# Performance work log

Hardware: AMD Instinct MI355X
Metric: run time of the kernel (lower is better)

## Reference

```python
import jax, jax.numpy as jnp
import numpy as np

COS_EPS = 1e-8  # torch F.cosine_similarity eps


def setup_inputs() -> dict:
    key = jax.random.key(0)
    k1, k2 = jax.random.split(key)
    x = jax.random.normal(k1, (8192, 512), dtype=jnp.float32)
    class_logits = jax.random.normal(k2, (8192, 100), dtype=jnp.float32)
    return {"x": x, "class_logits": class_logits}


def reference(x, class_logits):
    N, D = x.shape
    C = class_logits.shape[1]

    # class_logits.clone().detach()
    logits = jax.lax.stop_gradient(class_logits)
    pred = jax.nn.softmax(logits, axis=1)
    max_logit = pred.max(axis=1)          # [N]
    max_cls = pred.argmax(axis=1)         # [N] int

    # graph(): pairwise cosine similarity = normalize rows + gram matmul
    norms = jnp.linalg.norm(x, axis=1, keepdims=True)
    xn = x / jnp.maximum(norms, COS_EPS)
    mat = xn @ xn.T                       # [N, N]

    x_agg = mat @ x + x                   # [N, D]
    x_new = jax.lax.stop_gradient(x_agg)

    # update_prototype: per-class weighted scatter-add then mean over counts
    weighted = x_new * max_logit[:, None]                     # [N, D]
    sums = jax.ops.segment_sum(weighted, max_cls, num_segments=C)      # [C, D]
    counts = jax.ops.segment_sum(jnp.ones((N,), x.dtype), max_cls, num_segments=C)  # [C]
    prototypes = jnp.where(counts[:, None] > 0,
                           sums / jnp.maximum(counts, 1.0)[:, None],
                           jnp.zeros_like(sums))              # [C, D]

    # inter_class_matrix[i, j] = prototypes[j] - prototypes[i]
    inter_class_matrix = prototypes[None, :, :] - prototypes[:, None, :]  # [C, C, D]
    return prototypes, inter_class_matrix
```

## Files before the change

### kernel.cpp

```cpp
#include <hip/hip_runtime.h>
#include <math.h>

#define N_ROWS 8192
#define D_DIM  512
#define C_CLS  100

typedef unsigned short u16;
typedef unsigned int u32;
typedef __attribute__((ext_vector_type(8))) short short8;
typedef __attribute__((ext_vector_type(4))) float floatx4;

#define WS_G      0
#define WS_GP     262144
#define WS_INV    5505024
#define WS_SINV   5513216
#define WS_WV     5521408
#define WS_CLS    5529600
#define WS_CNT    5537792
#define WS_OFFS   5537920
#define WS_ORDER  5538048
#define WS_ZTH    5546240
#define WS_ZTL    7643392
#define WS_U      9740544
#define WS_V      9791744

__device__ __forceinline__ void split2(float v, u16& h, u16& l) {
    unsigned u = __float_as_uint(v);
    h = (u16)(u >> 16);
    float r = v - __uint_as_float(u & 0xFFFF0000u);
    l = (u16)(__float_as_uint(r) >> 16);
}

typedef const __attribute__((address_space(1))) u32* gp32;
typedef __attribute__((address_space(3))) u32* lp32;
__device__ __forceinline__ void cp16(const u16* g, u16* l) {
    __builtin_amdgcn_global_load_lds((gp32)g, (lp32)l, 16, 0, 0);
}

__global__ __launch_bounds__(256) void k_prep(const float* __restrict__ logits,
        const float* __restrict__ x, float* __restrict__ wv,
        int* __restrict__ cls, float* __restrict__ inv, float* __restrict__ sinv) {
    int wave = (blockIdx.x * blockDim.x + threadIdx.x) >> 6;
    int lane = threadIdx.x & 63;
    if (wave >= N_ROWS) return;
    const float* row = logits + (size_t)wave * C_CLS;
    float v1 = row[lane];
    bool has2 = (lane + 64) < C_CLS;
    float v2 = has2 ? row[lane + 64] : -INFINITY;
    float m; int idx;
    if (v2 > v1) { m = v2; idx = lane + 64; } else { m = v1; idx = lane; }
    #pragma unroll
    for (int off = 32; off >= 1; off >>= 1) {
        float om = __shfl_down(m, off);
        int   oi = __shfl_down(idx, off);
        if (om > m || (om == m && oi < idx)) { m = om; idx = oi; }
    }
    m = __shfl(m, 0);
    idx = __shfl(idx, 0);
    float s = expf(v1 - m) + (has2 ? expf(v2 - m) : 0.0f);
    #pragma unroll
    for (int off = 32; off >= 1; off >>= 1) s += __shfl_down(s, off);
    const float* xr = x + (size_t)wave * D_DIM;
    float ss = 0.f;
    #pragma unroll
    for (int j = 0; j < D_DIM; j += 64) {
        float v = xr[j + lane];
        ss += v * v;
    }
    #pragma unroll
    for (int off = 32; off >= 1; off >>= 1) ss += __shfl_down(ss, off);
    if (lane == 0) {
        wv[wave] = 1.0f / s;
        cls[wave] = idx;
        float iv = 1.0f / fmaxf(sqrtf(ss), 1e-8f);
        inv[wave] = iv;
        sinv[wave] = sqrtf(iv);
    }
}

#define LDT 65
__global__ __launch_bounds__(256) void k_mid(const float* __restrict__ x,
        const float* __restrict__ sinv, const int* __restrict__ cls,
        u16* __restrict__ zth, u16* __restrict__ ztl,
        int* __restrict__ cnt, int* __restrict__ offs, int* __restrict__ order) {
    __shared__ unsigned zt_p[64 * LDT];
    int bx = blockIdx.x;
    int t = threadIdx.x;
    if (bx == 1024) {
        __shared__ int hist[128], scan_s[128], cur[128];
        if (t < 128) hist[t] = 0;
        __syncthreads();
        for (int m2 = t; m2 < N_ROWS; m2 += 256) atomicAdd(&hist[cls[m2]], 1);
        __syncthreads();
        if (t < 128) scan_s[t] = hist[t];
        __syncthreads();
        #pragma unroll
        for (int d = 1; d < 128; d <<= 1) {
            int add = 0;
            if (t < 128 && t >= d) add = scan_s[t - d];
            __syncthreads();
            if (t < 128) scan_s[t] += add;
            __syncthreads();
        }
        if (t < 128) {
            int off0 = scan_s[t] - hist[t];
            cur[t] = off0;
            offs[t] = off0;
            cnt[t] = hist[t];
        }
        __syncthreads();
        for (int m2 = t; m2 < N_ROWS; m2 += 256) {
            int c2 = cls[m2];
            int p = atomicAdd(&cur[c2], 1);
            order[p] = m2;
        }
        return;
    }
    int r0 = (bx & 127) << 6, c0 = (bx >> 7) << 6;
    int r = t >> 2, cq = t & 3;
    const float* src = x + (size_t)(r0 + r) * D_DIM + c0 + cq * 16;
    float vv[16];
    {
        float4 a = *(const float4*)(src + 0);
        float4 b = *(const float4*)(src + 4);
        float4 c = *(const float4*)(src + 8);
        float4 d = *(const float4*)(src + 12);
        vv[0]=a.x; vv[1]=a.y; vv[2]=a.z; vv[3]=a.w;
        vv[4]=b.x; vv[5]=b.y; vv[6]=b.z; vv[7]=b.w;
        vv[8]=c.x; vv[9]=c.y; vv[10]=c.z; vv[11]=c.w;
        vv[12]=d.x; vv[13]=d.y; vv[14]=d.z; vv[15]=d.w;
    }
    float sv = sinv[r0 + r];
    #pragma unroll
    for (int j = 0; j < 16; ++j) {
        u16 h, l;
        split2(sv * vv[j], h, l);
        zt_p[(cq * 16 + j) * LDT + r] = ((unsigned)h << 16) | l;
    }
    __syncthreads();
    int c = t >> 2, rq = (t & 3) * 16;
    size_t tbase = (size_t)(c0 + c) * N_ROWS + r0 + rq;
    uint oh[8], ol[8];
    #pragma unroll
    for (int p = 0; p < 8; ++p) {
        unsigned d0 = zt_p[c * LDT + rq + 2*p];
        unsigned d1 = zt_p[c * LDT + rq + 2*p + 1];
        oh[p] = (d0 >> 16) | (d1 & 0xFFFF0000u);
        ol[p] = (d0 & 0xFFFFu) | (d1 << 16);
    }
    *(uint4*)&zth[tbase]     = make_uint4(oh[0], oh[1], oh[2], oh[3]);
    *(uint4*)&zth[tbase + 8] = make_uint4(oh[4], oh[5], oh[6], oh[7]);
    *(uint4*)&ztl[tbase]     = make_uint4(ol[0], ol[1], ol[2], ol[3]);
    *(uint4*)&ztl[tbase + 8] = make_uint4(ol[4], ol[5], ol[6], ol[7]);
}

__global__ __launch_bounds__(256) void k_big(const u16* __restrict__ zth,
        const u16* __restrict__ ztl, const float* __restrict__ x,
        const float* __restrict__ inv, const float* __restrict__ wv,
        const int* __restrict__ order, const int* __restrict__ offs,
        const int* __restrict__ cnt, float* __restrict__ Gp,
        float* __restrict__ u, float* __restrict__ v) {
    __shared__ __attribute__((aligned(16))) u16 Ah[128*32], Al[128*32];
    __shared__ __attribute__((aligned(16))) u16 Bh[128*32], Bl[128*32];
    __shared__ float us[4][64], vs[4][64];
    int bx = blockIdx.x;
    int t = threadIdx.x;
    if (bx >= 320) {
        int idx = bx - 320;
        int c = idx >> 3, jc = idx & 7;
        int g = t >> 6, lane = t & 63;
        int j = jc * 64 + lane;
        int n = cnt[c], o = offs[c];
        float ua = 0.f, va = 0.f;
        for (int p = g; p < n; p += 4) {
            int m = order[o + p];
            float wm = wv[m];
            float wi = wm * inv[m];
            float xv = x[(size_t)m * D_DIM + j];
            ua += wi * xv; va += wm * xv;
        }
        us[g][lane] = ua; vs[g][lane] = va;
        __syncthreads();
        if (g == 0) {
            u[(size_t)c * D_DIM + j] = us[0][lane] + us[1][lane] + us[2][lane] + us[3][lane];
            v[(size_t)c * D_DIM + j] = vs[0][lane] + vs[1][lane] + vs[2][lane] + vs[3][lane];
        }
        return;
    }
    int tile = bx % 10;
    int p = bx / 10;
    int ti = tile < 4 ? 0 : (tile < 7 ? 1 : (tile < 9 ? 2 : 3));
    int tj = tile - (ti == 0 ? 0 : (ti == 1 ? 3 : (ti == 2 ? 5 : 6)));
    int i0 = ti << 7, j0 = tj << 7;
    bool diag = (ti == tj);
    int kb = p << 8;
    int w = t >> 6, l = t & 63;
    int srow = t >> 2, scol = (t & 3) << 3;
    int lm = l & 15, lg = l >> 4;
    floatx4 acc[4][4];
    #pragma unroll
    for (int mi = 0; mi < 4; ++mi)
        #pragma unroll
        for (int ni = 0; ni < 4; ++ni) acc[mi][ni] = (floatx4){0.f,0.f,0.f,0.f};
    int d0 = srow * 32 + scol;
    int d1 = (64 + srow) * 32 + scol;
    const size_t ga0 = (size_t)(i0 + srow) * N_ROWS + kb + scol;
    const size_t ga1 = (size_t)(i0 + 64 + srow) * N_ROWS + kb + scol;
    const size_t gb0 = (size_t)(j0 + srow) * N_ROWS + kb + scol;
    const size_t gb1 = (size_t)(j0 + 64 + srow) * N_ROWS + kb + scol;
    const u16* Bhs = diag ? Ah : Bh;
    const u16* Bls = diag ? Al : Bl;
    for (int s = 0; s < 8; ++s) {
        int ks = s << 5;
        cp16(zth + ga0 + ks, Ah + d0);
        cp16(zth + ga1 + ks, Ah + d1);
        cp16(ztl + ga0 + ks, Al + d0);
        cp16(ztl + ga1 + ks, Al + d1);
        if (!diag) {
            cp16(zth + gb0 + ks, Bh + d0);
            cp16(zth + gb1 + ks, Bh + d1);
            cp16(ztl + gb0 + ks, Bl + d0);
            cp16(ztl + gb1 + ks, Bl + d1);
        }
        __syncthreads();
        short8 ah[4], al[4], bh[4], bl[4];
        #pragma unroll
        for (int mi = 0; mi < 4; ++mi) {
            int off = (((w & 1) << 6) + (mi << 4) + lm) * 32 + (lg << 3);
            ah[mi] = *(const short8*)&Ah[off];
            al[mi] = *(const short8*)&Al[off];
        }
        #pragma unroll
        for (int ni = 0; ni < 4; ++ni) {
            int off = (((w >> 1) << 6) + (ni << 4) + lm) * 32 + (lg << 3);
            bh[ni] = *(const short8*)&Bhs[off];
            bl[ni] = *(const short8*)&Bls[off];
        }
        #pragma unroll
        for (int mi = 0; mi < 4; ++mi)
            #pragma unroll
            for (int ni = 0; ni < 4; ++ni) {
                acc[mi][ni] = __builtin_amdgcn_mfma_f32_16x16x32_bf16(ah[mi], bh[ni], acc[mi][ni], 0, 0, 0);
                acc[mi][ni] = __builtin_amdgcn_mfma_f32_16x16x32_bf16(ah[mi], bl[ni], acc[mi][ni], 0, 0, 0);
                acc[mi][ni] = __builtin_amdgcn_mfma_f32_16x16x32_bf16(al[mi], bh[ni], acc[mi][ni], 0, 0, 0);
            }
        __syncthreads();
    }
    float* Gb = Gp + ((size_t)(p * 10 + tile) << 14);
    #pragma unroll
    for (int mi = 0; mi < 4; ++mi) {
        int row0 = ((w & 1) << 6) + (mi << 4) + (lg << 2);
        #pragma unroll
        for (int ni = 0; ni < 4; ++ni) {
            int col = ((w >> 1) << 6) + (ni << 4) + lm;
            #pragma unroll
            for (int r = 0; r < 4; ++r)
                Gb[(size_t)(row0 + r) * 128 + col] = acc[mi][ni][r];
        }
    }
}

__global__ void k_reduceG(const float* __restrict__ Gp, float* __restrict__ G) {
    int i = blockIdx.x * 256 + threadIdx.x;
    int r = i >> 9, c = i & 511;
    int tr = r >> 7, tc = c >> 7, rr = r & 127, cc = c & 127;
    if (tr > tc) { int tmp = tr; tr = tc; tc = tmp; tmp = rr; rr = cc; cc = tmp; }
    int tid = tr * 4 + tc - ((tr * (tr + 1)) >> 1);
    const float* src = Gp + ((size_t)tid << 14) + rr * 128 + cc;
    float s = 0.f;
    #pragma unroll
    for (int p = 0; p < 32; ++p) s += src[(size_t)p * 163840];
    G[i] = s;
}

__global__ __launch_bounds__(256) void k_pgemm(const float* __restrict__ u,
        const float* __restrict__ v, const int* __restrict__ cnt,
        const float* __restrict__ G, float* __restrict__ out) {
    __shared__ float us[D_DIM];
    int c = blockIdx.x >> 1;
    int j = ((blockIdx.x & 1) << 8) + threadIdx.x;
    us[threadIdx.x]       = u[(size_t)c * D_DIM + threadIdx.x];
    us[threadIdx.x + 256] = u[(size_t)c * D_DIM + threadIdx.x + 256];
    __syncthreads();
    float acc = v[(size_t)c * D_DIM + j];
    #pragma unroll 8
    for (int k = 0; k < D_DIM; ++k)
        acc += us[k] * G[(size_t)k * D_DIM + j];
    int n = cnt[c];
    float s = (n > 0) ? 1.0f / (float)n : 0.0f;
    out[(size_t)c * D_DIM + j] = acc * s;
}

__global__ void k_inter(const float* __restrict__ proto, float* __restrict__ out) {
    int pair = blockIdx.x;
    int i = pair / C_CLS;
    int j = pair - i * C_CLS;
    int d = threadIdx.x << 2;
    float4 pj = *(const float4*)&proto[j * D_DIM + d];
    float4 pi = *(const float4*)&proto[i * D_DIM + d];
    float4 r;
    r.x = pj.x - pi.x; r.y = pj.y - pi.y; r.z = pj.z - pi.z; r.w = pj.w - pi.w;
    *(float4*)&out[(size_t)pair * D_DIM + d] = r;
}

extern "C" void kernel_launch(void* const* d_in, const int* in_sizes, int n_in,
                              void* d_out, int out_size, void* d_ws, size_t ws_size,
                              hipStream_t stream) {
    const float* x      = (const float*)d_in[0];
    const float* logits = (const float*)d_in[1];
    float* out = (float*)d_out;
    float* ws  = (float*)d_ws;
    float* G     = ws + WS_G;
    float* Gp    = ws + WS_GP;
    float* inv   = ws + WS_INV;
    float* sinv  = ws + WS_SINV;
    float* wv    = ws + WS_WV;
    int*   cls   = (int*)(ws + WS_CLS);
    int*   cnt   = (int*)(ws + WS_CNT);
    int*   offs  = (int*)(ws + WS_OFFS);
    int*   order = (int*)(ws + WS_ORDER);
    u16* zth = (u16*)(ws + WS_ZTH);
    u16* ztl = (u16*)(ws + WS_ZTL);
    float* u_arr = ws + WS_U;
    float* v_arr = ws + WS_V;

    k_prep<<<N_ROWS / 4, 256, 0, stream>>>(logits, x, wv, cls, inv, sinv);
    k_mid<<<1025, 256, 0, stream>>>(x, sinv, cls, zth, ztl, cnt, offs, order);
    k_big<<<1120, 256, 0, stream>>>(zth, ztl, x, inv, wv, order, offs, cnt, Gp, u_arr, v_arr);
    k_reduceG<<<D_DIM * D_DIM / 256, 256, 0, stream>>>(Gp, G);
    k_pgemm<<<C_CLS * 2, 256, 0, stream>>>(u_arr, v_arr, cnt, G, out);
    k_inter<<<C_CLS * C_CLS, 128, 0, stream>>>(out, out + C_CLS * D_DIM);
}
```

Baseline: 178.8 us.

## Fuse all phases into one cooperative persistent kernel with grid syncs

Merges the six separate kernel launches into a single cooperative kernel of 256 persistent blocks that runs each phase in turn, separated by grid-wide syncs, with shared memory reused through a union. The Gram split-K is halved from 32 to 16 partitions, so each block does twice the K-work and the reduction reads fewer partials. The aim is to remove launch gaps and tail effects between the kernels. The cost is far less parallelism: the 1120-block GEMM becomes 160 MFMA blocks on a GPU with 256 CUs, and grid.sync adds its own overhead. A fallback path launches the same phases as separate kernels.

```diff
diff --git a/kernel.cpp b/kernel.cpp
--- a/kernel.cpp
+++ b/kernel.cpp
@@ -1,9 +1,13 @@
 #include <hip/hip_runtime.h>
+#include <hip/hip_cooperative_groups.h>
 #include <math.h>
+
+namespace cg = cooperative_groups;
 
 #define N_ROWS 8192
 #define D_DIM  512
 #define C_CLS  100
+#define GRID   256
 
 typedef unsigned short u16;
 typedef unsigned int u32;
@@ -12,17 +16,29 @@
 
 #define WS_G      0
 #define WS_GP     262144
-#define WS_INV    5505024
-#define WS_SINV   5513216
-#define WS_WV     5521408
-#define WS_CLS    5529600
-#define WS_CNT    5537792
-#define WS_OFFS   5537920
-#define WS_ORDER  5538048
-#define WS_ZTH    5546240
-#define WS_ZTL    7643392
-#define WS_U      9740544
-#define WS_V      9791744
+#define WS_INV    2883584
+#define WS_SINV   2891776
+#define WS_WV     2899968
+#define WS_CLS    2908160
+#define WS_CNT    2916352
+#define WS_OFFS   2916480
+#define WS_ORDER  2916608
+#define WS_ZTH    2924800
+#define WS_ZTL    5021952
+#define WS_U      7119104
+#define WS_V      7170304
+
+#define LDT 65
+
+struct SMem {
+    union {
+        struct { u16 Ah[128*32], Al[128*32], Bh[128*32], Bl[128*32]; } g;
+        unsigned zt_p[64 * LDT];
+        struct { int hist[128], scan[128], cur[128]; } s;
+        struct { float us[4][64], vs[4][64]; } uv;
+        float ug[D_DIM];
+    };
+};
 
 __device__ __forceinline__ void split2(float v, u16& h, u16& l) {
     unsigned u = __float_as_uint(v);
@@ -37,270 +53,324 @@
     __builtin_amdgcn_global_load_lds((gp32)g, (lp32)l, 16, 0, 0);
 }
 
-__global__ __launch_bounds__(256) void k_prep(const float* __restrict__ logits,
+__device__ void phase_prep(int bx, int t, const float* __restrict__ logits,
         const float* __restrict__ x, float* __restrict__ wv,
         int* __restrict__ cls, float* __restrict__ inv, float* __restrict__ sinv) {
-    int wave = (blockIdx.x * blockDim.x + threadIdx.x) >> 6;
-    int lane = threadIdx.x & 63;
-    if (wave >= N_ROWS) return;
-    const float* row = logits + (size_t)wave * C_CLS;
-    float v1 = row[lane];
-    bool has2 = (lane + 64) < C_CLS;
-    float v2 = has2 ? row[lane + 64] : -INFINITY;
-    float m; int idx;
-    if (v2 > v1) { m = v2; idx = lane + 64; } else { m = v1; idx = lane; }
-    #pragma unroll
-    for (int off = 32; off >= 1; off >>= 1) {
-        float om = __shfl_down(m, off);
-        int   oi = __shfl_down(idx, off);
-        if (om > m || (om == m && oi < idx)) { m = om; idx = oi; }
-    }
-    m = __shfl(m, 0);
-    idx = __shfl(idx, 0);
-    float s = expf(v1 - m) + (has2 ? expf(v2 - m) : 0.0f);
-    #pragma unroll
-    for (int off = 32; off >= 1; off >>= 1) s += __shfl_down(s, off);
-    const float* xr = x + (size_t)wave * D_DIM;
-    float ss = 0.f;
-    #pragma unroll
-    for (int j = 0; j < D_DIM; j += 64) {
-        float v = xr[j + lane];
-        ss += v * v;
-    }
-    #pragma unroll
-    for (int off = 32; off >= 1; off >>= 1) ss += __shfl_down(ss, off);
-    if (lane == 0) {
-        wv[wave] = 1.0f / s;
-        cls[wave] = idx;
-        float iv = 1.0f / fmaxf(sqrtf(ss), 1e-8f);
-        inv[wave] = iv;
-        sinv[wave] = sqrtf(iv);
-    }
-}
-
-#define LDT 65
-__global__ __launch_bounds__(256) void k_mid(const float* __restrict__ x,
+    int gwave = (bx << 2) + (t >> 6);
+    int lane = t & 63;
+    for (int row = gwave; row < N_ROWS; row += 1024) {
+        const float* lrow = logits + (size_t)row * C_CLS;
+        float v1 = lrow[lane];
+        bool has2 = (lane + 64) < C_CLS;
+        float v2 = has2 ? lrow[lane + 64] : -INFINITY;
+        float m; int idx;
+        if (v2 > v1) { m = v2; idx = lane + 64; } else { m = v1; idx = lane; }
+        #pragma unroll
+        for (int off = 32; off >= 1; off >>= 1) {
+            float om = __shfl_down(m, off);
+            int   oi = __shfl_down(idx, off);
+            if (om > m || (om == m && oi < idx)) { m = om; idx = oi; }
+        }
+        m = __shfl(m, 0);
+        idx = __shfl(idx, 0);
+        float s = expf(v1 - m) + (has2 ? expf(v2 - m) : 0.0f);
+        #pragma unroll
+        for (int off = 32; off >= 1; off >>= 1) s += __shfl_down(s, off);
+        const float* xr = x + (size_t)row * D_DIM;
+        float ss = 0.f;
+        #pragma unroll
+        for (int j = 0; j < D_DIM; j += 64) {
+            float v = xr[j + lane];
+            ss += v * v;
+        }
+        #pragma unroll
+        for (int off = 32; off >= 1; off >>= 1) ss += __shfl_down(ss, off);
+        if (lane == 0) {
+            wv[row] = 1.0f / s;
+            cls[row] = idx;
+            float iv = 1.0f / fmaxf(sqrtf(ss), 1e-8f);
+            inv[row] = iv;
+            sinv[row] = sqrtf(iv);
+        }
+    }
+}
+
+__device__ void phase_mid(SMem& sm, int bx, int t, const float* __restrict__ x,
         const float* __restrict__ sinv, const int* __restrict__ cls,
         u16* __restrict__ zth, u16* __restrict__ ztl,
         int* __restrict__ cnt, int* __restrict__ offs, int* __restrict__ order) {
-    __shared__ unsigned zt_p[64 * LDT];
-    int bx = blockIdx.x;
-    int t = threadIdx.x;
-    if (bx == 1024) {
-        __shared__ int hist[128], scan_s[128], cur[128];
-        if (t < 128) hist[t] = 0;
-        __syncthreads();
-        for (int m2 = t; m2 < N_ROWS; m2 += 256) atomicAdd(&hist[cls[m2]], 1);
-        __syncthreads();
-        if (t < 128) scan_s[t] = hist[t];
+    if (bx == GRID - 1) {
+        if (t < 128) sm.s.hist[t] = 0;
+        __syncthreads();
+        for (int m2 = t; m2 < N_ROWS; m2 += 256) atomicAdd(&sm.s.hist[cls[m2]], 1);
+        __syncthreads();
+        if (t < 128) sm.s.scan[t] = sm.s.hist[t];
         __syncthreads();
         #pragma unroll
         for (int d = 1; d < 128; d <<= 1) {
-            int add = 0;
-            if (t < 128 && t >= d) add = scan_s[t - d];
-            __syncthreads();
-            if (t < 128) scan_s[t] += add;
+            int add = (t < 128 && t >= d) ? sm.s.scan[t - d] : 0;
+            __syncthreads();
+            if (t < 128) sm.s.scan[t] += add;
             __syncthreads();
         }
         if (t < 128) {
-            int off0 = scan_s[t] - hist[t];
-            cur[t] = off0;
+            int off0 = sm.s.scan[t] - sm.s.hist[t];
+            sm.s.cur[t] = off0;
             offs[t] = off0;
-            cnt[t] = hist[t];
+            cnt[t] = sm.s.hist[t];
         }
         __syncthreads();
         for (int m2 = t; m2 < N_ROWS; m2 += 256) {
-            int c2 = cls[m2];
-            int p = atomicAdd(&cur[c2], 1);
+            int p = atomicAdd(&sm.s.cur[cls[m2]], 1);
             order[p] = m2;
         }
         return;
     }
-    int r0 = (bx & 127) << 6, c0 = (bx >> 7) << 6;
-    int r = t >> 2, cq = t & 3;
-    const float* src = x + (size_t)(r0 + r) * D_DIM + c0 + cq * 16;
-    float vv[16];
-    {
-        float4 a = *(const float4*)(src + 0);
-        float4 b = *(const float4*)(src + 4);
-        float4 c = *(const float4*)(src + 8);
-        float4 d = *(const float4*)(src + 12);
-        vv[0]=a.x; vv[1]=a.y; vv[2]=a.z; vv[3]=a.w;
-        vv[4]=b.x; vv[5]=b.y; vv[6]=b.z; vv[7]=b.w;
-        vv[8]=c.x; vv[9]=c.y; vv[10]=c.z; vv[11]=c.w;
-        vv[12]=d.x; vv[13]=d.y; vv[14]=d.z; vv[15]=d.w;
-    }
-    float sv = sinv[r0 + r];
-    #pragma unroll
-    for (int j = 0; j < 16; ++j) {
-        u16 h, l;
-        split2(sv * vv[j], h, l);
-        zt_p[(cq * 16 + j) * LDT + r] = ((unsigned)h << 16) | l;
-    }
-    __syncthreads();
-    int c = t >> 2, rq = (t & 3) * 16;
-    size_t tbase = (size_t)(c0 + c) * N_ROWS + r0 + rq;
-    uint oh[8], ol[8];
-    #pragma unroll
-    for (int p = 0; p < 8; ++p) {
-        unsigned d0 = zt_p[c * LDT + rq + 2*p];
-        unsigned d1 = zt_p[c * LDT + rq + 2*p + 1];
-        oh[p] = (d0 >> 16) | (d1 & 0xFFFF0000u);
-        ol[p] = (d0 & 0xFFFFu) | (d1 << 16);
-    }
-    *(uint4*)&zth[tbase]     = make_uint4(oh[0], oh[1], oh[2], oh[3]);
-    *(uint4*)&zth[tbase + 8] = make_uint4(oh[4], oh[5], oh[6], oh[7]);
-    *(uint4*)&ztl[tbase]     = make_uint4(ol[0], ol[1], ol[2], ol[3]);
-    *(uint4*)&ztl[tbase + 8] = make_uint4(ol[4], ol[5], ol[6], ol[7]);
-}
-
-__global__ __launch_bounds__(256) void k_big(const u16* __restrict__ zth,
+    for (int tile = bx; tile < 1024; tile += (GRID - 1)) {
+        int r0 = (tile & 127) << 6, c0 = (tile >> 7) << 6;
+        int r = t >> 2, cq = t & 3;
+        const float* src = x + (size_t)(r0 + r) * D_DIM + c0 + cq * 16;
+        float vv[16];
+        {
+            float4 a = *(const float4*)(src + 0);
+            float4 b = *(const float4*)(src + 4);
+            float4 c = *(const float4*)(src + 8);
+            float4 d = *(const float4*)(src + 12);
+            vv[0]=a.x; vv[1]=a.y; vv[2]=a.z; vv[3]=a.w;
+            vv[4]=b.x; vv[5]=b.y; vv[6]=b.z; vv[7]=b.w;
+            vv[8]=c.x; vv[9]=c.y; vv[10]=c.z; vv[11]=c.w;
+            vv[12]=d.x; vv[13]=d.y; vv[14]=d.z; vv[15]=d.w;
+        }
+        float sv = sinv[r0 + r];
+        #pragma unroll
+        for (int j = 0; j < 16; ++j) {
+            u16 h, l;
+            split2(sv * vv[j], h, l);
+            sm.zt_p[(cq * 16 + j) * LDT + r] = ((unsigned)h << 16) | l;
+        }
+        __syncthreads();
+        int c = t >> 2, rq = (t & 3) * 16;
+        size_t tbase = (size_t)(c0 + c) * N_ROWS + r0 + rq;
+        uint oh[8], ol[8];
+        #pragma unroll
+        for (int p = 0; p < 8; ++p) {
+            unsigned d0 = sm.zt_p[c * LDT + rq + 2*p];
+            unsigned d1 = sm.zt_p[c * LDT + rq + 2*p + 1];
+            oh[p] = (d0 >> 16) | (d1 & 0xFFFF0000u);
+            ol[p] = (d0 & 0xFFFFu) | (d1 << 16);
+        }
+        *(uint4*)&zth[tbase]     = make_uint4(oh[0], oh[1], oh[2], oh[3]);
+        *(uint4*)&zth[tbase + 8] = make_uint4(oh[4], oh[5], oh[6], oh[7]);
+        *(uint4*)&ztl[tbase]     = make_uint4(ol[0], ol[1], ol[2], ol[3]);
+        *(uint4*)&ztl[tbase + 8] = make_uint4(ol[4], ol[5], ol[6], ol[7]);
+        __syncthreads();
+    }
+}
+
+__device__ void phase_big(SMem& sm, int bx, int t, const u16* __restrict__ zth,
         const u16* __restrict__ ztl, const float* __restrict__ x,
         const float* __restrict__ inv, const float* __restrict__ wv,
         const int* __restrict__ order, const int* __restrict__ offs,
         const int* __restrict__ cnt, float* __restrict__ Gp,
-        float* __restrict__ u, float* __restrict__ v) {
-    __shared__ __attribute__((aligned(16))) u16 Ah[128*32], Al[128*32];
-    __shared__ __attribute__((aligned(16))) u16 Bh[128*32], Bl[128*32];
-    __shared__ float us[4][64], vs[4][64];
-    int bx = blockIdx.x;
-    int t = threadIdx.x;
-    if (bx >= 320) {
-        int idx = bx - 320;
-        int c = idx >> 3, jc = idx & 7;
-        int g = t >> 6, lane = t & 63;
-        int j = jc * 64 + lane;
-        int n = cnt[c], o = offs[c];
-        float ua = 0.f, va = 0.f;
-        for (int p = g; p < n; p += 4) {
-            int m = order[o + p];
-            float wm = wv[m];
-            float wi = wm * inv[m];
-            float xv = x[(size_t)m * D_DIM + j];
-            ua += wi * xv; va += wm * xv;
-        }
-        us[g][lane] = ua; vs[g][lane] = va;
-        __syncthreads();
-        if (g == 0) {
-            u[(size_t)c * D_DIM + j] = us[0][lane] + us[1][lane] + us[2][lane] + us[3][lane];
-            v[(size_t)c * D_DIM + j] = vs[0][lane] + vs[1][lane] + vs[2][lane] + vs[3][lane];
-        }
-        return;
-    }
-    int tile = bx % 10;
-    int p = bx / 10;
-    int ti = tile < 4 ? 0 : (tile < 7 ? 1 : (tile < 9 ? 2 : 3));
-    int tj = tile - (ti == 0 ? 0 : (ti == 1 ? 3 : (ti == 2 ? 5 : 6)));
-    int i0 = ti << 7, j0 = tj << 7;
-    bool diag = (ti == tj);
-    int kb = p << 8;
-    int w = t >> 6, l = t & 63;
-    int srow = t >> 2, scol = (t & 3) << 3;
-    int lm = l & 15, lg = l >> 4;
-    floatx4 acc[4][4];
-    #pragma unroll
-    for (int mi = 0; mi < 4; ++mi)
-        #pragma unroll
-        for (int ni = 0; ni < 4; ++ni) acc[mi][ni] = (floatx4){0.f,0.f,0.f,0.f};
-    int d0 = srow * 32 + scol;
-    int d1 = (64 + srow) * 32 + scol;
-    const size_t ga0 = (size_t)(i0 + srow) * N_ROWS + kb + scol;
-    const size_t ga1 = (size_t)(i0 + 64 + srow) * N_ROWS + kb + scol;
-    const size_t gb0 = (size_t)(j0 + srow) * N_ROWS + kb + scol;
-    const size_t gb1 = (size_t)(j0 + 64 + srow) * N_ROWS + kb + scol;
-    const u16* Bhs = diag ? Ah : Bh;
-    const u16* Bls = diag ? Al : Bl;
-    for (int s = 0; s < 8; ++s) {
-        int ks = s << 5;
-        cp16(zth + ga0 + ks, Ah + d0);
-        cp16(zth + ga1 + ks, Ah + d1);
-        cp16(ztl + ga0 + ks, Al + d0);
-        cp16(ztl + ga1 + ks, Al + d1);
-        if (!diag) {
-            cp16(zth + gb0 + ks, Bh + d0);
-            cp16(zth + gb1 + ks, Bh + d1);
-            cp16(ztl + gb0 + ks, Bl + d0);
-            cp16(ztl + gb1 + ks, Bl + d1);
-        }
-        __syncthreads();
-        short8 ah[4], al[4], bh[4], bl[4];
-        #pragma unroll
-        for (int mi = 0; mi < 4; ++mi) {
-            int off = (((w & 1) << 6) + (mi << 4) + lm) * 32 + (lg << 3);
-            ah[mi] = *(const short8*)&Ah[off];
-            al[mi] = *(const short8*)&Al[off];
-        }
-        #pragma unroll
-        for (int ni = 0; ni < 4; ++ni) {
-            int off = (((w >> 1) << 6) + (ni << 4) + lm) * 32 + (lg << 3);
-            bh[ni] = *(const short8*)&Bhs[off];
-            bl[ni] = *(const short8*)&Bls[off];
-        }
+        float* __restrict__ u_arr, float* __restrict__ v_arr) {
+    if (bx < 160) {
+        int tile = bx % 10;
+        int p = bx / 10;
+        int ti = tile < 4 ? 0 : (tile < 7 ? 1 : (tile < 9 ? 2 : 3));
+        int tj = tile - (ti == 0 ? 0 : (ti == 1 ? 3 : (ti == 2 ? 5 : 6)));
+        int i0 = ti << 7, j0 = tj << 7;
+        bool diag = (ti == tj);
+        int kb = p << 9;
+        int w = t >> 6, l = t & 63;
+        int srow = t >> 2, scol = (t & 3) << 3;
+        int lm = l & 15, lg = l >> 4;
+        floatx4 acc[4][4];
         #pragma unroll
         for (int mi = 0; mi < 4; ++mi)
             #pragma unroll
+            for (int ni = 0; ni < 4; ++ni) acc[mi][ni] = (floatx4){0.f,0.f,0.f,0.f};
+        int d0 = srow * 32 + scol;
+        int d1 = (64 + srow) * 32 + scol;
+        const size_t ga0 = (size_t)(i0 + srow) * N_ROWS + kb + scol;
+        const size_t ga1 = (size_t)(i0 + 64 + srow) * N_ROWS + kb + scol;
+        const size_t gb0 = (size_t)(j0 + srow) * N_ROWS + kb + scol;
+        const size_t gb1 = (size_t)(j0 + 64 + srow) * N_ROWS + kb + scol;
+        const u16* Bhs = diag ? sm.g.Ah : sm.g.Bh;
+        const u16* Bls = diag ? sm.g.Al : sm.g.Bl;
+        for (int s = 0; s < 16; ++s) {
+            int ks = s << 5;
+            cp16(zth + ga0 + ks, sm.g.Ah + d0);
+            cp16(zth + ga1 + ks, sm.g.Ah + d1);
+            cp16(ztl + ga0 + ks, sm.g.Al + d0);
+            cp16(ztl + ga1 + ks, sm.g.Al + d1);
+            if (!diag) {
+                cp16(zth + gb0 + ks, sm.g.Bh + d0);
+                cp16(zth + gb1 + ks, sm.g.Bh + d1);
+                cp16(ztl + gb0 + ks, sm.g.Bl + d0);
+                cp16(ztl + gb1 + ks, sm.g.Bl + d1);
+            }
+            __syncthreads();
+            short8 ah[4], al[4], bh[4], bl[4];
+            #pragma unroll
+            for (int mi = 0; mi < 4; ++mi) {
+                int off = (((w & 1) << 6) + (mi << 4) + lm) * 32 + (lg << 3);
+                ah[mi] = *(const short8*)&sm.g.Ah[off];
+                al[mi] = *(const short8*)&sm.g.Al[off];
+            }
+            #pragma unroll
             for (int ni = 0; ni < 4; ++ni) {
-                acc[mi][ni] = __builtin_amdgcn_mfma_f32_16x16x32_bf16(ah[mi], bh[ni], acc[mi][ni], 0, 0, 0);
-                acc[mi][ni] = __builtin_amdgcn_mfma_f32_16x16x32_bf16(ah[mi], bl[ni], acc[mi][ni], 0, 0, 0);
-                acc[mi][ni] = __builtin_amdgcn_mfma_f32_16x16x32_bf16(al[mi], bh[ni], acc[mi][ni], 0, 0, 0);
-            }
-        __syncthreads();
-    }
-    float* Gb = Gp + ((size_t)(p * 10 + tile) << 14);
+                int off = (((w >> 1) << 6) + (ni << 4) + lm) * 32 + (lg << 3);
+                bh[ni] = *(const short8*)&Bhs[off];
+                bl[ni] = *(const short8*)&Bls[off];
+            }
+            #pragma unroll
+            for (int mi = 0; mi < 4; ++mi)
+                #pragma unroll
+                for (int ni = 0; ni < 4; ++ni) {
+                    acc[mi][ni] = __builtin_amdgcn_mfma_f32_16x16x32_bf16(ah[mi], bh[ni], acc[mi][ni], 0, 0, 0);
+                    acc[mi][ni] = __builtin_amdgcn_mfma_f32_16x16x32_bf16(ah[mi], bl[ni], acc[mi][ni], 0, 0, 0);
+                    acc[mi][ni] = __builtin_amdgcn_mfma_f32_16x16x32_bf16(al[mi], bh[ni], acc[mi][ni], 0, 0, 0);
+                }
+            __syncthreads();
+        }
+        float* Gb = Gp + ((size_t)(p * 10 + tile) << 14);
+        #pragma unroll
+        for (int mi = 0; mi < 4; ++mi) {
+            int row0 = ((w & 1) << 6) + (mi << 4) + (lg << 2);
+            #pragma unroll
+            for (int ni = 0; ni < 4; ++ni) {
+                int col = ((w >> 1) << 6) + (ni << 4) + lm;
+                #pragma unroll
+                for (int r = 0; r < 4; ++r)
+                    Gb[(size_t)(row0 + r) * 128 + col] = acc[mi][ni][r];
+            }
+        }
+    } else {
+        for (int idx = bx - 160; idx < 800; idx += (GRID - 160)) {
+            int c = idx >> 3, jc = idx & 7;
+            int g = t >> 6, lane = t & 63;
+            int j = jc * 64 + lane;
+            int n = cnt[c], o = offs[c];
+            float ua = 0.f, va = 0.f;
+            for (int p = g; p < n; p += 4) {
+                int m = order[o + p];
+                float wm = wv[m];
+                float wi = wm * inv[m];
+                float xv = x[(size_t)m * D_DIM + j];
+                ua += wi * xv; va += wm * xv;
+            }
+            sm.uv.us[g][lane] = ua; sm.uv.vs[g][lane] = va;
+            __syncthreads();
+            if (g == 0) {
+                u_arr[(size_t)c * D_DIM + j] = sm.uv.us[0][lane] + sm.uv.us[1][lane] + sm.uv.us[2][lane] + sm.uv.us[3][lane];
+                v_arr[(size_t)c * D_DIM + j] = sm.uv.vs[0][lane] + sm.uv.vs[1][lane] + sm.uv.vs[2][lane] + sm.uv.vs[3][lane];
+            }
+            __syncthreads();
+        }
+    }
+}
+
+__device__ void phase_reduceG(int bx, int t, const float* __restrict__ Gp,
+                              float* __restrict__ G) {
+    int base = bx * 256 + t;
     #pragma unroll
-    for (int mi = 0; mi < 4; ++mi) {
-        int row0 = ((w & 1) << 6) + (mi << 4) + (lg << 2);
-        #pragma unroll
-        for (int ni = 0; ni < 4; ++ni) {
-            int col = ((w >> 1) << 6) + (ni << 4) + lm;
-            #pragma unroll
-            for (int r = 0; r < 4; ++r)
-                Gb[(size_t)(row0 + r) * 128 + col] = acc[mi][ni][r];
-        }
-    }
-}
-
-__global__ void k_reduceG(const float* __restrict__ Gp, float* __restrict__ G) {
-    int i = blockIdx.x * 256 + threadIdx.x;
-    int r = i >> 9, c = i & 511;
-    int tr = r >> 7, tc = c >> 7, rr = r & 127, cc = c & 127;
-    if (tr > tc) { int tmp = tr; tr = tc; tc = tmp; tmp = rr; rr = cc; cc = tmp; }
-    int tid = tr * 4 + tc - ((tr * (tr + 1)) >> 1);
-    const float* src = Gp + ((size_t)tid << 14) + rr * 128 + cc;
-    float s = 0.f;
-    #pragma unroll
-    for (int p = 0; p < 32; ++p) s += src[(size_t)p * 163840];
-    G[i] = s;
-}
-
-__global__ __launch_bounds__(256) void k_pgemm(const float* __restrict__ u,
-        const float* __restrict__ v, const int* __restrict__ cnt,
+    for (int q = 0; q < 4; ++q) {
+        int i = base + q * 65536;
+        int r = i >> 9, c = i & 511;
+        int tr = r >> 7, tc = c >> 7, rr = r & 127, cc = c & 127;
+        if (tr > tc) { int tmp = tr; tr = tc; tc = tmp; tmp = rr; rr = cc; cc = tmp; }
+        int tid = tr * 4 + tc - ((tr * (tr + 1)) >> 1);
+        const float* src = Gp + ((size_t)tid << 14) + rr * 128 + cc;
+        float ssum = 0.f;
+        #pragma unroll
+        for (int p = 0; p < 16; ++p) ssum += src[(size_t)p * 163840];
+        G[i] = ssum;
+    }
+}
+
+__device__ void phase_pgemm(SMem& sm, int bx, int t, const float* __restrict__ u_arr,
+        const float* __restrict__ v_arr, const int* __restrict__ cnt,
         const float* __restrict__ G, float* __restrict__ out) {
-    __shared__ float us[D_DIM];
-    int c = blockIdx.x >> 1;
-    int j = ((blockIdx.x & 1) << 8) + threadIdx.x;
-    us[threadIdx.x]       = u[(size_t)c * D_DIM + threadIdx.x];
-    us[threadIdx.x + 256] = u[(size_t)c * D_DIM + threadIdx.x + 256];
+    if (bx >= 2 * C_CLS) return;
+    int c = bx >> 1;
+    int j = ((bx & 1) << 8) + t;
+    sm.ug[t]       = u_arr[(size_t)c * D_DIM + t];
+    sm.ug[t + 256] = u_arr[(size_t)c * D_DIM + t + 256];
     __syncthreads();
-    float acc = v[(size_t)c * D_DIM + j];
+    float acc = v_arr[(size_t)c * D_DIM + j];
     #pragma unroll 8
     for (int k = 0; k < D_DIM; ++k)
-        acc += us[k] * G[(size_t)k * D_DIM + j];
+        acc += sm.ug[k] * G[(size_t)k * D_DIM + j];
     int n = cnt[c];
     float s = (n > 0) ? 1.0f / (float)n : 0.0f;
     out[(size_t)c * D_DIM + j] = acc * s;
 }
 
-__global__ void k_inter(const float* __restrict__ proto, float* __restrict__ out) {
-    int pair = blockIdx.x;
-    int i = pair / C_CLS;
-    int j = pair - i * C_CLS;
-    int d = threadIdx.x << 2;
-    float4 pj = *(const float4*)&proto[j * D_DIM + d];
-    float4 pi = *(const float4*)&proto[i * D_DIM + d];
-    float4 r;
-    r.x = pj.x - pi.x; r.y = pj.y - pi.y; r.z = pj.z - pi.z; r.w = pj.w - pi.w;
-    *(float4*)&out[(size_t)pair * D_DIM + d] = r;
+__device__ void phase_inter(int bx, int t, const float* __restrict__ proto,
+                            float* __restrict__ inter) {
+    for (int pp = bx * 2; pp < C_CLS * C_CLS; pp += GRID * 2) {
+        int pair = pp + (t >> 7);
+        int i = pair / C_CLS;
+        int j = pair - i * C_CLS;
+        int d = (t & 127) << 2;
+        float4 pj = *(const float4*)&proto[j * D_DIM + d];
+        float4 pi = *(const float4*)&proto[i * D_DIM + d];
+        float4 r;
+        r.x = pj.x - pi.x; r.y = pj.y - pi.y; r.z = pj.z - pi.z; r.w = pj.w - pi.w;
+        *(float4*)&inter[(size_t)pair * D_DIM + d] = r;
+    }
+}
+
+__global__ __launch_bounds__(256, 2) void k_all(
+        const float* __restrict__ x, const float* __restrict__ logits,
+        float* __restrict__ wv, int* __restrict__ cls,
+        float* __restrict__ inv, float* __restrict__ sinv,
+        u16* __restrict__ zth, u16* __restrict__ ztl,
+        int* __restrict__ cnt, int* __restrict__ offs, int* __restrict__ order,
+        float* __restrict__ Gp, float* __restrict__ u_arr, float* __restrict__ v_arr,
+        float* __restrict__ G, float* __restrict__ out) {
+    cg::grid_group grid = cg::this_grid();
+    __shared__ SMem sm;
+    int bx = blockIdx.x, t = threadIdx.x;
+    phase_prep(bx, t, logits, x, wv, cls, inv, sinv);
+    grid.sync();
+    phase_mid(sm, bx, t, x, sinv, cls, zth, ztl, cnt, offs, order);
+    grid.sync();
+    phase_big(sm, bx, t, zth, ztl, x, inv, wv, order, offs, cnt, Gp, u_arr, v_arr);
+    grid.sync();
+    phase_reduceG(bx, t, Gp, G);
+    grid.sync();
+    phase_pgemm(sm, bx, t, u_arr, v_arr, cnt, G, out);
+    grid.sync();
+    phase_inter(bx, t, out, out + C_CLS * D_DIM);
+}
+
+__global__ __launch_bounds__(256) void k_p1(const float* x, const float* logits,
+        float* wv, int* cls, float* inv, float* sinv) {
+    phase_prep(blockIdx.x, threadIdx.x, logits, x, wv, cls, inv, sinv);
+}
+__global__ __launch_bounds__(256) void k_p2(const float* x, const float* sinv,
+        const int* cls, u16* zth, u16* ztl, int* cnt, int* offs, int* order) {
+    __shared__ SMem sm;
+    phase_mid(sm, blockIdx.x, threadIdx.x, x, sinv, cls, zth, ztl, cnt, offs, order);
+}
+__global__ __launch_bounds__(256) void k_p3(const u16* zth, const u16* ztl,
+        const float* x, const float* inv, const float* wv, const int* order,
+        const int* offs, const int* cnt, float* Gp, float* u_arr, float* v_arr) {
+    __shared__ SMem sm;
+    phase_big(sm, blockIdx.x, threadIdx.x, zth, ztl, x, inv, wv, order, offs, cnt,
+              Gp, u_arr, v_arr);
+}
+__global__ __launch_bounds__(256) void k_p4(const float* Gp, float* G) {
+    phase_reduceG(blockIdx.x, threadIdx.x, Gp, G);
+}
+__global__ __launch_bounds__(256) void k_p5(const float* u_arr, const float* v_arr,
+        const int* cnt, const float* G, float* out) {
+    __shared__ SMem sm;
+    phase_pgemm(sm, blockIdx.x, threadIdx.x, u_arr, v_arr, cnt, G, out);
+}
+__global__ __launch_bounds__(256) void k_p6(const float* proto, float* inter) {
+    phase_inter(blockIdx.x, threadIdx.x, proto, inter);
 }
 
 extern "C" void kernel_launch(void* const* d_in, const int* in_sizes, int n_in,
@@ -324,10 +394,21 @@
     float* u_arr = ws + WS_U;
     float* v_arr = ws + WS_V;
 
-    k_prep<<<N_ROWS / 4, 256, 0, stream>>>(logits, x, wv, cls, inv, sinv);
-    k_mid<<<1025, 256, 0, stream>>>(x, sinv, cls, zth, ztl, cnt, offs, order);
-    k_big<<<1120, 256, 0, stream>>>(zth, ztl, x, inv, wv, order, offs, cnt, Gp, u_arr, v_arr);
-    k_reduceG<<<D_DIM * D_DIM / 256, 256, 0, stream>>>(Gp, G);
-    k_pgemm<<<C_CLS * 2, 256, 0, stream>>>(u_arr, v_arr, cnt, G, out);
-    k_inter<<<C_CLS * C_CLS, 128, 0, stream>>>(out, out + C_CLS * D_DIM);
-}
+    void* args[] = {
+        (void*)&x, (void*)&logits, (void*)&wv, (void*)&cls, (void*)&inv,
+        (void*)&sinv, (void*)&zth, (void*)&ztl, (void*)&cnt, (void*)&offs,
+        (void*)&order, (void*)&Gp, (void*)&u_arr, (void*)&v_arr, (void*)&G,
+        (void*)&out
+    };
+    hipError_t err = hipLaunchCooperativeKernel((void*)k_all, dim3(GRID), dim3(256),
+                                                args, 0, stream);
+    if (err != hipSuccess) {
+        k_p1<<<GRID, 256, 0, stream>>>(x, logits, wv, cls, inv, sinv);
+        k_p2<<<GRID, 256, 0, stream>>>(x, sinv, cls, zth, ztl, cnt, offs, order);
+        k_p3<<<GRID, 256, 0, stream>>>(zth, ztl, x, inv, wv, order, offs, cnt,
+                                       Gp, u_arr, v_arr);
+        k_p4<<<GRID, 256, 0, stream>>>(Gp, G);
+        k_p5<<<GRID, 256, 0, stream>>>(u_arr, v_arr, cnt, G, out);
+        k_p6<<<GRID, 256, 0, stream>>>(out, out + C_CLS * D_DIM);
+    }
+}
```

Result: slower. 355.3 us (+98.7%).
